# Optimization experiments

Hardware: AMD Instinct MI355X
Metric: run time of the kernel (lower is better)

Reference implementation:

```python
import jax, jax.numpy as jnp
import numpy as np
import math

NUM_CONVS = 4
GN_GROUPS = 32
GN_EPS = 1e-5
FPN_STRIDES = (8, 16, 32, 64, 128)
PRIOR_PROB = 0.01


def conv3x3(x, w, b):
    # x: [N,C,H,W], w: [O,I,3,3]
    y = jax.lax.conv_general_dilated(
        x, w, window_strides=(1, 1), padding='SAME',
        dimension_numbers=('NCHW', 'OIHW', 'NCHW'))
    return y + b[None, :, None, None]


def group_norm(x, gamma, beta):
    n, c, h, w = x.shape
    xg = x.reshape(n, GN_GROUPS, c // GN_GROUPS, h, w)
    mean = xg.mean(axis=(2, 3, 4), keepdims=True)
    var = xg.var(axis=(2, 3, 4), keepdims=True)
    xn = ((xg - mean) * jax.lax.rsqrt(var + GN_EPS)).reshape(n, c, h, w)
    return xn * gamma[None, :, None, None] + beta[None, :, None, None]


def subnet(x, ws, bs, gws, gbs):
    # NUM_CONVS x (conv3x3 -> GN -> ReLU)
    for i in range(NUM_CONVS):
        x = jax.nn.relu(group_norm(conv3x3(x, ws[i], bs[i]), gws[i], gbs[i]))
    return x


def permute_to_N_HWA_K(x, k):
    n = x.shape[0]
    return x.transpose(0, 2, 3, 1).reshape(n, -1, k)


def setup_inputs() -> dict:
    key = jax.random.key(0)
    ks = jax.random.split(key, 16)
    C, K = 256, 80
    feats = {
        'p3': jax.random.normal(ks[0], (1, C, 80, 80), jnp.float32),
        'p4': jax.random.normal(ks[1], (1, C, 40, 40), jnp.float32),
        'p5': jax.random.normal(ks[2], (1, C, 20, 20), jnp.float32),
        'p6': jax.random.normal(ks[3], (1, C, 10, 10), jnp.float32),
        'p7': jax.random.normal(ks[4], (1, C, 5, 5), jnp.float32),
    }
    std = 0.01
    bias_value = -math.log((1 - PRIOR_PROB) / PRIOR_PROB)
    params = {
        'cls_w': std * jax.random.normal(ks[5], (NUM_CONVS, C, C, 3, 3), jnp.float32),
        'cls_b': jnp.zeros((NUM_CONVS, C), jnp.float32),
        'cls_gn_w': jnp.ones((NUM_CONVS, C), jnp.float32),
        'cls_gn_b': jnp.zeros((NUM_CONVS, C), jnp.float32),
        'box_w': std * jax.random.normal(ks[6], (NUM_CONVS, C, C, 3, 3), jnp.float32),
        'box_b': jnp.zeros((NUM_CONVS, C), jnp.float32),
        'box_gn_w': jnp.ones((NUM_CONVS, C), jnp.float32),
        'box_gn_b': jnp.zeros((NUM_CONVS, C), jnp.float32),
        'score_w': std * jax.random.normal(ks[7], (K, C, 3, 3), jnp.float32),
        'score_b': jnp.full((K,), bias_value, jnp.float32),
        'pred_w': std * jax.random.normal(ks[8], (4, C, 3, 3), jnp.float32),
        'pred_b': jnp.zeros((4,), jnp.float32),
        'iou_w': std * jax.random.normal(ks[9], (1, C, 3, 3), jnp.float32),
        'iou_b': jnp.zeros((1,), jnp.float32),
        'scales': jnp.ones((5,), jnp.float32),
    }
    return {**feats, **params}


def reference(p3, p4, p5, p6, p7,
              cls_w, cls_b, cls_gn_w, cls_gn_b,
              box_w, box_b, box_gn_w, box_gn_b,
              score_w, score_b, pred_w, pred_b, iou_w, iou_b, scales):
    features = [p3, p4, p5, p6, p7]
    logits, bbox_reg, ious = [], [], []
    for l, feat in enumerate(features):
        c = subnet(feat, cls_w, cls_b, cls_gn_w, cls_gn_b)
        b = subnet(feat, box_w, box_b, box_gn_w, box_gn_b)
        logit = conv3x3(c, score_w, score_b)          # [N,80,H,W]
        iou = conv3x3(b, iou_w, iou_b)                # [N,1,H,W]
        bp = conv3x3(b, pred_w, pred_b) * scales[l]   # Scale module
        # norm_reg_targets=True branch
        reg = jax.nn.relu(bp) * FPN_STRIDES[l]        # [N,4,H,W]
        logits.append(permute_to_N_HWA_K(logit, 80))
        bbox_reg.append(permute_to_N_HWA_K(reg, 4))
        ious.append(permute_to_N_HWA_K(iou, 1))
    box_cls = jnp.concatenate(logits, axis=1)    # [N, sumHW, 80]
    box_delta = jnp.concatenate(bbox_reg, axis=1)  # [N, sumHW, 4]
    box_iou = jnp.concatenate(ious, axis=1)      # [N, sumHW, 1]
    # pack into one array for a single output: [N, sumHW, 85]
    return jnp.concatenate([box_cls, box_delta, box_iou], axis=-1)
```

## Files before the change

kernel.cpp:

```cpp
#include <hip/hip_runtime.h>

typedef unsigned short u16;
typedef __attribute__((ext_vector_type(8))) short bf16x8;
typedef __attribute__((ext_vector_type(4))) float f32x4;

#define NLEV 5
#define CCH 256
#define KTOT 2304
#define P_TOT 8525
#define PP_TOT 9165

__constant__ int   c_HW[NLEV]     = {6400, 1600, 400, 100, 25};
__constant__ int   c_W[NLEV]      = {80, 40, 20, 10, 5};
__constant__ int   c_off[NLEV]    = {0, 6400, 8000, 8400, 8500};
__constant__ int   c_poff[NLEV]   = {0, 6724, 8488, 8972, 9116};
__constant__ int   c_pts[NLEV+1]  = {0, 200, 250, 263, 267, 268};
__constant__ float c_stridef[NLEV]= {8.f, 16.f, 32.f, 64.f, 128.f};

__device__ __forceinline__ u16 f2bf(float f){
  union { float f; unsigned u; } v; v.f = f;
  unsigned r = v.u + 0x7fffu + ((v.u >> 16) & 1u);
  return (u16)(r >> 16);
}

__device__ __forceinline__ void g2l16(const u16* g, u16* l, int lane){
#if defined(__has_builtin)
#if __has_builtin(__builtin_amdgcn_global_load_lds)
  __builtin_amdgcn_global_load_lds(
      (const __attribute__((address_space(1))) unsigned int*)g,
      (__attribute__((address_space(3))) unsigned int*)l, 16, 0, 0);
  return;
#endif
#endif
  *(uint4*)(l + lane*8) = *(const uint4*)g;
}

template<int MODE>
__global__ __launch_bounds__(256, 4) void gemm_conv(
    const u16* __restrict__ Xc, const u16* __restrict__ Xb,
    const u16* __restrict__ Wc, const u16* __restrict__ Wb,
    const float* __restrict__ bc, const float* __restrict__ bb,
    float* __restrict__ Yc, float* __restrict__ Yb,
    float* __restrict__ stats,
    const float* __restrict__ predb, const float* __restrict__ ioub,
    const float* __restrict__ scales, float* __restrict__ out)
{
  __shared__ u16 sA[128*64];
  __shared__ u16 sB[32*64];
  __shared__ float sstat[16][2];

  const int ptile = blockIdx.x, mtile = blockIdx.y, br = blockIdx.z;
  int lv = 0;
  #pragma unroll
  for (int i = 1; i < NLEV; i++) if (ptile >= c_pts[i]) lv = i;
  const int ptl = ptile - c_pts[lv];
  const int HW = c_HW[lv], Wl = c_W[lv], wrow = Wl + 2;
  const int tid = threadIdx.x, wv = tid >> 6, ln = tid & 63;
  const int quad = ln >> 4, l15 = ln & 15;
  const int lr = ln >> 3;
  const int gsw = (ln & 7) ^ lr;

  const u16* __restrict__ X  = br ? Xb : Xc;
  const u16* __restrict__ WA = br ? Wb : Wc;

  const u16* asrc[4]; u16* adst[4];
  #pragma unroll
  for (int j = 0; j < 4; j++) {
    const int row = wv*32 + j*8;
    asrc[j] = WA + (size_t)(mtile*128 + row + lr) * KTOT + gsw*8;
    adst[j] = &sA[row * 64];
  }
  const u16* bsrc; u16* bdst;
  {
    const int p = ptl*32 + wv*8 + lr;
    int pb = 0;
    if (p < HW) { const int h = p / Wl, wi = p - h*Wl; pb = h*wrow + wi; }
    bsrc = X + (size_t)(c_poff[lv] + pb) * CCH + gsw*8;
    bdst = &sB[(wv*8) * 64];
  }

  const u16 *afp[2][2], *bfp[2][2];
  #pragma unroll
  for (int sub = 0; sub < 2; sub++) {
    const int gb = ((sub*4 + quad) ^ (l15 & 7)) * 8;
    #pragma unroll
    for (int mt = 0; mt < 2; mt++)
      afp[sub][mt] = &sA[(wv*32 + mt*16 + l15)*64 + gb];
    #pragma unroll
    for (int nt = 0; nt < 2; nt++)
      bfp[sub][nt] = &sB[(nt*16 + l15)*64 + gb];
  }

  f32x4 acc[2][2];
  #pragma unroll
  for (int i = 0; i < 2; i++)
    #pragma unroll
    for (int j = 0; j < 2; j++) acc[i][j] = (f32x4){0.f, 0.f, 0.f, 0.f};

  for (int s = 0; s < 36; s++) {
    const int tap = s >> 2;
    const int dh = tap / 3, dw = tap - dh*3;
    const int aof = s * 64;
    const int bof = (dh*wrow + dw)*CCH + ((s & 3) << 6);
    #pragma unroll
    for (int j = 0; j < 4; j++) g2l16(asrc[j] + aof, adst[j], ln);
    g2l16(bsrc + bof, bdst, ln);
    __syncthreads();
    bf16x8 af[2][2], bf[2][2];
    #pragma unroll
    for (int sub = 0; sub < 2; sub++) {
      #pragma unroll
      for (int mt = 0; mt < 2; mt++) af[sub][mt] = *(const bf16x8*)afp[sub][mt];
      #pragma unroll
      for (int nt = 0; nt < 2; nt++) bf[sub][nt] = *(const bf16x8*)bfp[sub][nt];
    }
    #pragma unroll
    for (int sub = 0; sub < 2; sub++)
      #pragma unroll
      for (int mt = 0; mt < 2; mt++)
        #pragma unroll
        for (int nt = 0; nt < 2; nt++)
          acc[mt][nt] = __builtin_amdgcn_mfma_f32_16x16x32_bf16(
              af[sub][mt], bf[sub][nt], acc[mt][nt], 0, 0, 0);
    __syncthreads();
  }

  const int nrem = HW - ptl*32;
  if (MODE == 0) {
    if (tid < 32) sstat[tid >> 1][tid & 1] = 0.f;
    __syncthreads();
    const float* __restrict__ bias = br ? bb : bc;
    float* __restrict__ Y = br ? Yb : Yc;
    #pragma unroll
    for (int mt = 0; mt < 2; mt++) {
      const int mloc = wv*32 + mt*16 + quad*4;
      const int mrow = mtile*128 + mloc;
      const f32x4 bv = *(const f32x4*)&bias[mrow];
      float s = 0.f, sq = 0.f;
      #pragma unroll
      for (int nt = 0; nt < 2; nt++) {
        const int nl = nt*16 + l15;
        f32x4 v = acc[mt][nt] + bv;
        if (nl < nrem) {
          const size_t n = (size_t)(c_off[lv] + ptl*32 + nl);
          *(f32x4*)&Y[n*CCH + mrow] = v;
          #pragma unroll
          for (int r = 0; r < 4; r++) { s += v[r]; sq += v[r]*v[r]; }
        }
      }
      #pragma unroll
      for (int o = 1; o < 16; o <<= 1) { s += __shfl_xor(s, o); sq += __shfl_xor(sq, o); }
      if (l15 == 0) {
        const int g = mloc >> 3;
        atomicAdd(&sstat[g][0], s);
        atomicAdd(&sstat[g][1], sq);
      }
    }
    __syncthreads();
    if (tid < 32) {
      const int g = tid >> 1, c = tid & 1;
      atomicAdd(&stats[((br*NLEV + lv)*32 + mtile*16 + g)*2 + c], sstat[g][c]);
    }
  } else {
    const float scl = scales[lv];
    const float stf = c_stridef[lv];
    #pragma unroll
    for (int mt = 0; mt < 2; mt++) {
      const int mr0 = wv*32 + mt*16 + quad*4;
      if (mr0 >= 85) continue;
      #pragma unroll
      for (int nt = 0; nt < 2; nt++) {
        const int nl = nt*16 + l15;
        if (nl >= nrem) continue;
        const size_t n = (size_t)(c_off[lv] + ptl*32 + nl);
        const f32x4 v = acc[mt][nt];
        #pragma unroll
        for (int r = 0; r < 4; r++) {
          const int m = mr0 + r;
          if (br == 0) {
            if (m < 80) out[n*85 + m] = v[r] + bc[m];
          } else {
            if (m < 4) {
              const float t = (v[r] + predb[m]) * scl;
              out[n*85 + 80 + m] = fmaxf(t, 0.f) * stf;
            } else if (m == 4) {
              out[n*85 + 84] = v[r] + ioub[0];
            }
          }
        }
      }
    }
  }
}

__global__ __launch_bounds__(256) void gn_relu(
    const float* __restrict__ Yc, const float* __restrict__ Yb,
    const float* __restrict__ stats,
    const float* __restrict__ gwc, const float* __restrict__ gbc,
    const float* __restrict__ gwb, const float* __restrict__ gbb,
    u16* __restrict__ Xc, u16* __restrict__ Xb)
{
  const int t = blockIdx.x * 256 + threadIdx.x;
  if (t >= 2 * P_TOT * 32) return;
  const int br = t / (P_TOT * 32);
  const int r  = t - br * (P_TOT * 32);
  const int pg = r >> 5;
  const int c0 = (r & 31) << 3;
  int lv = 0;
  #pragma unroll
  for (int i = 1; i < NLEV; i++) if (pg >= c_off[i]) lv = i;
  const int pl = pg - c_off[lv];
  const int Wl = c_W[lv];
  const int g = c0 >> 3;
  const float* st = &stats[(((size_t)br*NLEV + lv)*32 + g)*2];
  const float cnt = 8.f * (float)c_HW[lv];
  const float mean = st[0] / cnt;
  const float var  = st[1] / cnt - mean*mean;
  const float rstd = rsqrtf(var + 1e-5f);
  const float* Y  = br ? Yb : Yc;
  const float* gw = br ? gwb : gwc;
  const float* gb = br ? gbb : gbc;
  u16* X = br ? Xb : Xc;
  const float* y = &Y[(size_t)pg*CCH + c0];
  const int h = pl / Wl, wi = pl - h*Wl;
  const size_t pidx = (size_t)(c_poff[lv] + (h+1)*(Wl+2) + (wi+1));
  union { u16 u[8]; uint4 v; } pk;
  #pragma unroll
  for (int i = 0; i < 8; i++) {
    const float v = (y[i] - mean)*rstd*gw[c0+i] + gb[c0+i];
    pk.u[i] = f2bf(fmaxf(v, 0.f));
  }
  *(uint4*)&X[pidx*CCH + c0] = pk.v;
}

__global__ __launch_bounds__(256) void feat2bf(
    const float* __restrict__ p3, const float* __restrict__ p4,
    const float* __restrict__ p5, const float* __restrict__ p6,
    const float* __restrict__ p7, u16* __restrict__ X)
{
  const int t = blockIdx.x * 256 + threadIdx.x;
  if (t >= P_TOT * 32) return;
  const int pg = t >> 5, c0 = (t & 31) << 3;
  int lv = 0;
  #pragma unroll
  for (int i = 1; i < NLEV; i++) if (pg >= c_off[i]) lv = i;
  const int pl = pg - c_off[lv];
  const float* src = lv==0 ? p3 : lv==1 ? p4 : lv==2 ? p5 : lv==3 ? p6 : p7;
  const int HW = c_HW[lv], Wl = c_W[lv];
  const int h = pl / Wl, wi = pl - h*Wl;
  const size_t pidx = (size_t)(c_poff[lv] + (h+1)*(Wl+2) + (wi+1));
  union { u16 u[8]; uint4 v; } pk;
  #pragma unroll
  for (int i = 0; i < 8; i++)
    pk.u[i] = f2bf(src[(size_t)(c0+i)*HW + pl]);
  *(uint4*)&X[pidx*CCH + c0] = pk.v;
}

__global__ __launch_bounds__(256) void wconv(
    const float* __restrict__ cw, const float* __restrict__ bw,
    u16* __restrict__ Wc, u16* __restrict__ Wb)
{
  const size_t N = (size_t)4*256*KTOT;
  const size_t t = (size_t)blockIdx.x * 256 + threadIdx.x;
  if (t >= 2*N) return;
  const float* src = (t < N) ? cw : bw;
  u16* dst = (t < N) ? Wc : Wb;
  const size_t i = (t < N) ? t : t - N;
  const size_t lc = i / KTOT;
  const int kk = (int)(i - lc*KTOT);
  const int tap = kk >> 8, ci = kk & 255;
  dst[i] = f2bf(src[(lc*256 + ci)*9 + tap]);
}

__global__ __launch_bounds__(256) void hconv(
    const float* __restrict__ sw, const float* __restrict__ pw,
    const float* __restrict__ iw, u16* __restrict__ Whc, u16* __restrict__ Whb)
{
  const int N = 128 * KTOT;
  const int t = blockIdx.x * 256 + threadIdx.x;
  if (t >= 2*N) return;
  const int i = (t < N) ? t : t - N;
  const int co = i / KTOT, kk = i - co*KTOT;
  const int tap = kk >> 8, ci = kk & 255;
  float v = 0.f;
  if (t < N) {
    if (co < 80) v = sw[(co*256 + ci)*9 + tap];
    Whc[i] = f2bf(v);
  } else {
    if (co < 4)       v = pw[(co*256 + ci)*9 + tap];
    else if (co == 4) v = iw[ci*9 + tap];
    Whb[i] = f2bf(v);
  }
}

extern "C" void kernel_launch(void* const* d_in, const int* in_sizes, int n_in,
                              void* d_out, int out_size, void* d_ws, size_t ws_size,
                              hipStream_t stream)
{
  const float* p3      = (const float*)d_in[0];
  const float* p4      = (const float*)d_in[1];
  const float* p5      = (const float*)d_in[2];
  const float* p6      = (const float*)d_in[3];
  const float* p7      = (const float*)d_in[4];
  const float* cls_w   = (const float*)d_in[5];
  const float* cls_b   = (const float*)d_in[6];
  const float* cls_gw  = (const float*)d_in[7];
  const float* cls_gb  = (const float*)d_in[8];
  const float* box_w   = (const float*)d_in[9];
  const float* box_b   = (const float*)d_in[10];
  const float* box_gw  = (const float*)d_in[11];
  const float* box_gb  = (const float*)d_in[12];
  const float* score_w = (const float*)d_in[13];
  const float* score_b = (const float*)d_in[14];
  const float* pred_w  = (const float*)d_in[15];
  const float* pred_b  = (const float*)d_in[16];
  const float* iou_w   = (const float*)d_in[17];
  const float* iou_b   = (const float*)d_in[18];
  const float* scales  = (const float*)d_in[19];
  float* out = (float*)d_out;

  char* w = (char*)d_ws;
  size_t o = 0;
  auto alloc = [&](size_t b) { void* p = w + o; o += (b + 255) & ~(size_t)255; return p; };
  u16*   XF = (u16*)alloc((size_t)PP_TOT*CCH*2);
  u16*   XC = (u16*)alloc((size_t)PP_TOT*CCH*2);
  u16*   XB = (u16*)alloc((size_t)PP_TOT*CCH*2);
  float* ST = (float*)alloc((size_t)4*2*NLEV*32*2*4);
  u16*  WRC = (u16*)alloc((size_t)4*256*KTOT*2);
  u16*  WRB = (u16*)alloc((size_t)4*256*KTOT*2);
  u16*  WHC = (u16*)alloc((size_t)128*KTOT*2);
  u16*  WHB = (u16*)alloc((size_t)128*KTOT*2);
  float* YC = (float*)alloc((size_t)P_TOT*CCH*4);
  float* YB = (float*)alloc((size_t)P_TOT*CCH*4);

  hipMemsetAsync(XF, 0, (size_t)3*PP_TOT*CCH*2 + (size_t)4*2*NLEV*32*2*4, stream);

  wconv<<<dim3((unsigned)(((size_t)2*4*256*KTOT + 255)/256)), 256, 0, stream>>>(cls_w, box_w, WRC, WRB);
  hconv<<<dim3((2*128*KTOT + 255)/256), 256, 0, stream>>>(score_w, pred_w, iou_w, WHC, WHB);
  feat2bf<<<dim3((P_TOT*32 + 255)/256), 256, 0, stream>>>(p3, p4, p5, p6, p7, XF);

  const u16* xci = XF; const u16* xbi = XF;
  for (int l = 0; l < 4; l++) {
    float* STl = ST + (size_t)l*2*NLEV*32*2;
    gemm_conv<0><<<dim3(268, 2, 2), 256, 0, stream>>>(
        xci, xbi, WRC + (size_t)l*256*KTOT, WRB + (size_t)l*256*KTOT,
        cls_b + l*256, box_b + l*256, YC, YB, STl,
        nullptr, nullptr, nullptr, nullptr);
    gn_relu<<<dim3((2*P_TOT*32 + 255)/256), 256, 0, stream>>>(
        YC, YB, STl, cls_gw + l*256, cls_gb + l*256, box_gw + l*256, box_gb + l*256,
        XC, XB);
    xci = XC; xbi = XB;
  }
  gemm_conv<1><<<dim3(268, 1, 2), 256, 0, stream>>>(
      xci, xbi, WHC, WHB, score_b, nullptr, nullptr, nullptr, nullptr,
      pred_b, iou_b, scales, out);
}
```

Measured before the change: 389.6 us.

## Give each wave a private 64x64 tile and drop block-wide barriers in conv GEMM

Each block now covers all 256 output channels for 64 pixels, and every wave computes its own 64x64 output tile from a private LDS region. This replaces the shared 128x32 tile and the per-stage __syncthreads with per-wave s_waitcnt waits, and loads the next K-stage right after the current fragments are read from LDS so the fetch overlaps the MFMAs. The goal is more MFMA work per LDS read, no barrier stalls, and no duplicated per-block setup across the split over M. In exchange the grid shrinks to about one block per CU at lower occupancy, and each wave refetches the same B tile on its own. The head pass also exits early for waves whose output rows are not needed.

```diff
diff --git a/kernel.cpp b/kernel.cpp
--- a/kernel.cpp
+++ b/kernel.cpp
@@ -14,7 +14,7 @@
 __constant__ int   c_W[NLEV]      = {80, 40, 20, 10, 5};
 __constant__ int   c_off[NLEV]    = {0, 6400, 8000, 8400, 8500};
 __constant__ int   c_poff[NLEV]   = {0, 6724, 8488, 8972, 9116};
-__constant__ int   c_pts[NLEV+1]  = {0, 200, 250, 263, 267, 268};
+__constant__ int   c_pts[NLEV+1]  = {0, 100, 125, 132, 134, 135};
 __constant__ float c_stridef[NLEV]= {8.f, 16.f, 32.f, 64.f, 128.f};
 
 __device__ __forceinline__ u16 f2bf(float f){
@@ -35,8 +35,11 @@
   *(uint4*)(l + lane*8) = *(const uint4*)g;
 }
 
+#define WAIT_VM0   0x0F70
+#define WAIT_LGKM0 0xC07F
+
 template<int MODE>
-__global__ __launch_bounds__(256, 4) void gemm_conv(
+__global__ __launch_bounds__(256, 2) void gemm_conv(
     const u16* __restrict__ Xc, const u16* __restrict__ Xb,
     const u16* __restrict__ Wc, const u16* __restrict__ Wb,
     const float* __restrict__ bc, const float* __restrict__ bb,
@@ -45,17 +48,21 @@
     const float* __restrict__ predb, const float* __restrict__ ioub,
     const float* __restrict__ scales, float* __restrict__ out)
 {
-  __shared__ u16 sA[128*64];
-  __shared__ u16 sB[32*64];
-  __shared__ float sstat[16][2];
-
-  const int ptile = blockIdx.x, mtile = blockIdx.y, br = blockIdx.z;
+  __shared__ u16 sbuf[4*8192];
+  __shared__ float sstat[32][2];
+
+  const int ptile = blockIdx.x, br = blockIdx.z;
+  const int tid = threadIdx.x, wv = tid >> 6, ln = tid & 63;
+
+  if (MODE == 1) {
+    if (br == 0 ? (wv >= 2) : (wv >= 1)) return;
+  }
+
   int lv = 0;
   #pragma unroll
   for (int i = 1; i < NLEV; i++) if (ptile >= c_pts[i]) lv = i;
   const int ptl = ptile - c_pts[lv];
   const int HW = c_HW[lv], Wl = c_W[lv], wrow = Wl + 2;
-  const int tid = threadIdx.x, wv = tid >> 6, ln = tid & 63;
   const int quad = ln >> 4, l15 = ln & 15;
   const int lr = ln >> 3;
   const int gsw = (ln & 7) ^ lr;
@@ -63,86 +70,81 @@
   const u16* __restrict__ X  = br ? Xb : Xc;
   const u16* __restrict__ WA = br ? Wb : Wc;
 
-  const u16* asrc[4]; u16* adst[4];
-  #pragma unroll
-  for (int j = 0; j < 4; j++) {
-    const int row = wv*32 + j*8;
-    asrc[j] = WA + (size_t)(mtile*128 + row + lr) * KTOT + gsw*8;
-    adst[j] = &sA[row * 64];
-  }
-  const u16* bsrc; u16* bdst;
-  {
-    const int p = ptl*32 + wv*8 + lr;
+  u16* myA = &sbuf[wv * 8192];
+  u16* myB = myA + 4096;
+
+  const u16* aptr[8]; const u16* bptr[8];
+  #pragma unroll
+  for (int j = 0; j < 8; j++)
+    aptr[j] = WA + (size_t)(wv*64 + j*8 + lr) * KTOT + gsw*8;
+  #pragma unroll
+  for (int j = 0; j < 8; j++) {
+    const int p = ptl*64 + j*8 + lr;
     int pb = 0;
     if (p < HW) { const int h = p / Wl, wi = p - h*Wl; pb = h*wrow + wi; }
-    bsrc = X + (size_t)(c_poff[lv] + pb) * CCH + gsw*8;
-    bdst = &sB[(wv*8) * 64];
-  }
-
-  const u16 *afp[2][2], *bfp[2][2];
-  #pragma unroll
-  for (int sub = 0; sub < 2; sub++) {
-    const int gb = ((sub*4 + quad) ^ (l15 & 7)) * 8;
-    #pragma unroll
-    for (int mt = 0; mt < 2; mt++)
-      afp[sub][mt] = &sA[(wv*32 + mt*16 + l15)*64 + gb];
-    #pragma unroll
-    for (int nt = 0; nt < 2; nt++)
-      bfp[sub][nt] = &sB[(nt*16 + l15)*64 + gb];
-  }
-
-  f32x4 acc[2][2];
-  #pragma unroll
-  for (int i = 0; i < 2; i++)
-    #pragma unroll
-    for (int j = 0; j < 2; j++) acc[i][j] = (f32x4){0.f, 0.f, 0.f, 0.f};
-
-  for (int s = 0; s < 36; s++) {
+    bptr[j] = X + (size_t)(c_poff[lv] + pb) * CCH + gsw*8;
+  }
+
+  auto stage = [&](int s) {
     const int tap = s >> 2;
     const int dh = tap / 3, dw = tap - dh*3;
     const int aof = s * 64;
     const int bof = (dh*wrow + dw)*CCH + ((s & 3) << 6);
     #pragma unroll
-    for (int j = 0; j < 4; j++) g2l16(asrc[j] + aof, adst[j], ln);
-    g2l16(bsrc + bof, bdst, ln);
-    __syncthreads();
-    bf16x8 af[2][2], bf[2][2];
+    for (int j = 0; j < 8; j++) g2l16(aptr[j] + aof, myA + j*512, ln);
+    #pragma unroll
+    for (int j = 0; j < 8; j++) g2l16(bptr[j] + bof, myB + j*512, ln);
+  };
+
+  f32x4 acc[4][4];
+  #pragma unroll
+  for (int i = 0; i < 4; i++)
+    #pragma unroll
+    for (int j = 0; j < 4; j++) acc[i][j] = (f32x4){0.f, 0.f, 0.f, 0.f};
+
+  stage(0);
+  #pragma unroll 1
+  for (int s = 0; s < 36; s++) {
+    __builtin_amdgcn_s_waitcnt(WAIT_VM0);
+    bf16x8 af[2][4], bf[2][4];
     #pragma unroll
     for (int sub = 0; sub < 2; sub++) {
-      #pragma unroll
-      for (int mt = 0; mt < 2; mt++) af[sub][mt] = *(const bf16x8*)afp[sub][mt];
-      #pragma unroll
-      for (int nt = 0; nt < 2; nt++) bf[sub][nt] = *(const bf16x8*)bfp[sub][nt];
+      const int ga = ((sub*4 + quad) ^ (l15 & 7)) * 8;
+      #pragma unroll
+      for (int t = 0; t < 4; t++) {
+        af[sub][t] = *(const bf16x8*)&myA[(t*16 + l15)*64 + ga];
+        bf[sub][t] = *(const bf16x8*)&myB[(t*16 + l15)*64 + ga];
+      }
     }
+    __builtin_amdgcn_s_waitcnt(WAIT_LGKM0);
+    if (s < 35) stage(s + 1);
     #pragma unroll
     for (int sub = 0; sub < 2; sub++)
       #pragma unroll
-      for (int mt = 0; mt < 2; mt++)
+      for (int mt = 0; mt < 4; mt++)
         #pragma unroll
-        for (int nt = 0; nt < 2; nt++)
+        for (int nt = 0; nt < 4; nt++)
           acc[mt][nt] = __builtin_amdgcn_mfma_f32_16x16x32_bf16(
               af[sub][mt], bf[sub][nt], acc[mt][nt], 0, 0, 0);
-    __syncthreads();
-  }
-
-  const int nrem = HW - ptl*32;
+  }
+
+  const int nrem = HW - ptl*64;
   if (MODE == 0) {
-    if (tid < 32) sstat[tid >> 1][tid & 1] = 0.f;
+    if (tid < 64) sstat[tid >> 1][tid & 1] = 0.f;
     __syncthreads();
     const float* __restrict__ bias = br ? bb : bc;
     float* __restrict__ Y = br ? Yb : Yc;
     #pragma unroll
-    for (int mt = 0; mt < 2; mt++) {
-      const int mloc = wv*32 + mt*16 + quad*4;
-      const int mrow = mtile*128 + mloc;
+    for (int mt = 0; mt < 4; mt++) {
+      const int mrow = wv*64 + mt*16 + quad*4;
       const f32x4 bv = *(const f32x4*)&bias[mrow];
       float s = 0.f, sq = 0.f;
       #pragma unroll
-      for (int nt = 0; nt < 2; nt++) {
+      for (int nt = 0; nt < 4; nt++) {
         const int nl = nt*16 + l15;
         f32x4 v = acc[mt][nt] + bv;
         if (nl < nrem) {
-          const size_t n = (size_t)(c_off[lv] + ptl*32 + nl);
+          const size_t n = (size_t)(c_off[lv] + ptl*64 + nl);
           *(f32x4*)&Y[n*CCH + mrow] = v;
           #pragma unroll
           for (int r = 0; r < 4; r++) { s += v[r]; sq += v[r]*v[r]; }
@@ -151,28 +153,28 @@
       #pragma unroll
       for (int o = 1; o < 16; o <<= 1) { s += __shfl_xor(s, o); sq += __shfl_xor(sq, o); }
       if (l15 == 0) {
-        const int g = mloc >> 3;
+        const int g = mrow >> 3;
         atomicAdd(&sstat[g][0], s);
         atomicAdd(&sstat[g][1], sq);
       }
     }
     __syncthreads();
-    if (tid < 32) {
+    if (tid < 64) {
       const int g = tid >> 1, c = tid & 1;
-      atomicAdd(&stats[((br*NLEV + lv)*32 + mtile*16 + g)*2 + c], sstat[g][c]);
+      atomicAdd(&stats[((br*NLEV + lv)*32 + g)*2 + c], sstat[g][c]);
     }
   } else {
     const float scl = scales[lv];
     const float stf = c_stridef[lv];
     #pragma unroll
-    for (int mt = 0; mt < 2; mt++) {
-      const int mr0 = wv*32 + mt*16 + quad*4;
+    for (int mt = 0; mt < 4; mt++) {
+      const int mr0 = wv*64 + mt*16 + quad*4;
       if (mr0 >= 85) continue;
       #pragma unroll
-      for (int nt = 0; nt < 2; nt++) {
+      for (int nt = 0; nt < 4; nt++) {
         const int nl = nt*16 + l15;
         if (nl >= nrem) continue;
-        const size_t n = (size_t)(c_off[lv] + ptl*32 + nl);
+        const size_t n = (size_t)(c_off[lv] + ptl*64 + nl);
         const f32x4 v = acc[mt][nt];
         #pragma unroll
         for (int r = 0; r < 4; r++) {
@@ -342,7 +344,7 @@
   const u16* xci = XF; const u16* xbi = XF;
   for (int l = 0; l < 4; l++) {
     float* STl = ST + (size_t)l*2*NLEV*32*2;
-    gemm_conv<0><<<dim3(268, 2, 2), 256, 0, stream>>>(
+    gemm_conv<0><<<dim3(135, 1, 2), 256, 0, stream>>>(
         xci, xbi, WRC + (size_t)l*256*KTOT, WRB + (size_t)l*256*KTOT,
         cls_b + l*256, box_b + l*256, YC, YB, STl,
         nullptr, nullptr, nullptr, nullptr);
@@ -351,7 +353,7 @@
         XC, XB);
     xci = XC; xbi = XB;
   }
-  gemm_conv<1><<<dim3(268, 1, 2), 256, 0, stream>>>(
+  gemm_conv<1><<<dim3(135, 1, 2), 256, 0, stream>>>(
       xci, xbi, WHC, WHB, score_b, nullptr, nullptr, nullptr, nullptr,
       pred_b, iou_b, scales, out);
 }
```

New measurement: 396.6 us. Within noise of the previous version (+1.8%).
